# Performance work log

Hardware: AMD Instinct MI355X
Metric: run time of the kernel (lower is better)

Reference implementation:

```python
import jax, jax.numpy as jnp
import numpy as np

V_TH = 1.0  # spikingjelly IFNode default threshold; v starts at 0, hard reset after fire


def setup_inputs() -> dict:
    key = jax.random.key(0)
    k_x, k_w1, k_w2 = jax.random.split(key, 3)
    B, IN, FEAT, OUT = 4096, 3136, 6272, 500
    # binary input spikes (LatencyEncoder emits 0/1 spikes per timestep)
    x = (jax.random.uniform(k_x, (B, IN)) < 0.5).astype(jnp.float32)
    # Linear weights, torch layout [out_features, in_features], kaiming-ish scale
    W1 = jax.random.normal(k_w1, (FEAT, IN), dtype=jnp.float32) / np.sqrt(IN)
    W2 = jax.random.normal(k_w2, (OUT, FEAT), dtype=jnp.float32) / np.sqrt(FEAT)
    return {"x": x, "W1": W1, "W2": W2}


def reference(x, W1, W2):
    # Linear (no bias) -> IF neuron single step: v = 0 + I; spike = (v >= V_TH); hard reset
    v1 = x @ W1.T                      # [B, FEAT]
    s1 = (v1 >= V_TH).astype(x.dtype)  # binary hidden spikes
    v2 = s1 @ W2.T                     # [B, OUT]
    s2 = (v2 >= V_TH).astype(x.dtype)  # output spikes
    return s2
```

## Files before the change

### kernel.cpp

```cpp
#include <hip/hip_runtime.h>


namespace {
constexpr int kB = 4096;
constexpr int kIn = 3136;
constexpr int kFeat = 6272;
constexpr int kFeatWords = 196;
constexpr int kOut = 500;
constexpr size_t kPlane1 = (size_t)kFeat * kIn;
constexpr size_t kW1F = 3 * kPlane1;
constexpr size_t kW2F = (size_t)784 * 12288;
constexpr size_t kS1Bytes = (size_t)kB * kFeatWords * 4;
constexpr size_t kXb2Bytes = (size_t)49 * kB * 8;
constexpr unsigned kCap1 = 2u << 20;
constexpr unsigned kCap2 = 1u << 16;
__device__ constexpr double kTau1 = 7.4769e-4;
__device__ constexpr double kTau2 = 1.4955e-3;
}

typedef int v4i __attribute__((ext_vector_type(4)));
typedef int v16i __attribute__((ext_vector_type(16)));

__device__ __forceinline__ void gload_lds16(const void* g, void* l) {
  __builtin_amdgcn_global_load_lds((__attribute__((address_space(1))) void*)(g),
                                   (__attribute__((address_space(3))) void*)(l),
                                   16, 0, 0);
}

__device__ __forceinline__ v4i expand16(unsigned b) {
  unsigned u0 = (((b      ) & 0xFu) * 0x204081u) & 0x01010101u;
  unsigned u1 = (((b >> 4 ) & 0xFu) * 0x204081u) & 0x01010101u;
  unsigned u2 = (((b >> 8 ) & 0xFu) * 0x204081u) & 0x01010101u;
  unsigned u3 = (((b >> 12) & 0xFu) * 0x204081u) & 0x01010101u;
  return (v4i){(int)u0, (int)u1, (int)u2, (int)u3};
}

__device__ __forceinline__ void split3(float w, signed char* d) {
  float c = rintf(w * 128.f);
  d[0] = (signed char)(int)c;
  float r = fmaf(c, -7.8125e-03f, w);
  c = rintf(r * 16384.f);
  d[1] = (signed char)(int)c;
  r = fmaf(c, -6.103515625e-05f, r);
  c = rintf(r * 2097152.f);
  d[2] = (signed char)(int)c;
}

__global__ __launch_bounds__(256) void conv_w1F(const float* __restrict__ W,
                                                signed char* __restrict__ F) {
  const int bx = blockIdx.x;
  const int fb = bx / 49;
  const int kt = bx % 49;
  const int f = threadIdx.x & 63;
  const int g = threadIdx.x >> 6;
  const float* src = W + (size_t)(fb * 64 + f) * kIn + kt * 64 + g * 16;
  union { signed char c[16]; int4 v; } o[3];
#pragma unroll
  for (int q = 0; q < 4; ++q) {
    const float4 w = *(const float4*)(src + q * 4);
    signed char d[4][3];
    split3(w.x, d[0]); split3(w.y, d[1]); split3(w.z, d[2]); split3(w.w, d[3]);
#pragma unroll
    for (int e = 0; e < 4; ++e)
#pragma unroll
      for (int j = 0; j < 3; ++j) o[j].c[q * 4 + e] = d[e][j];
  }
#pragma unroll
  for (int j = 0; j < 3; ++j)
    *(int4*)(F + ((size_t)bx * 3 + j) * 4096 + g * 1024 + f * 16) = o[j].v;
}

__global__ __launch_bounds__(256) void conv_w2F(const float* __restrict__ W,
                                                signed char* __restrict__ F) {
  const int bx = blockIdx.x;
  const int fb = bx / 98;
  const int kt = bx % 98;
  const int f = threadIdx.x & 63;
  const int g = threadIdx.x >> 6;
  const int feat = fb * 64 + f;
  union { signed char c[16]; int4 v; } o[3];
#pragma unroll
  for (int q = 0; q < 4; ++q) {
    float4 w = {0.f, 0.f, 0.f, 0.f};
    if (feat < kOut)
      w = *(const float4*)(W + (size_t)feat * kFeat + kt * 64 + g * 16 + q * 4);
    signed char d[4][3];
    split3(w.x, d[0]); split3(w.y, d[1]); split3(w.z, d[2]); split3(w.w, d[3]);
#pragma unroll
    for (int e = 0; e < 4; ++e)
#pragma unroll
      for (int j = 0; j < 3; ++j) o[j].c[q * 4 + e] = d[e][j];
  }
#pragma unroll
  for (int j = 0; j < 3; ++j)
    *(int4*)(F + ((size_t)bx * 3 + j) * 4096 + g * 1024 + f * 16) = o[j].v;
}

__global__ __launch_bounds__(256) void pack_x2(const float* __restrict__ X,
                                               uint2* __restrict__ xb2) {
  const int wid = (blockIdx.x * 256 + threadIdx.x) >> 6;
  const int lane = threadIdx.x & 63;
  const int b = wid / 49;
  const int g = wid % 49;
  const float v = X[(size_t)b * kIn + g * 64 + lane];
  const unsigned long long bal = __ballot(v != 0.f);
  if (lane == 0) xb2[(size_t)g * kB + b] = make_uint2((unsigned)bal, (unsigned)(bal >> 32));
}

__global__ __launch_bounds__(512, 4) void fc1_v6(
    const uint2* __restrict__ xb2, const signed char* __restrict__ w1lF,
    unsigned* __restrict__ s1b, unsigned* __restrict__ s1T,
    unsigned* __restrict__ cnt, unsigned* __restrict__ list) {
  __shared__ __align__(16) signed char lds[24576];
  const int tid = threadIdx.x;
  const int lane = tid & 63;
  const int ln31 = lane & 31;
  const int half = lane >> 5;
  const int wv = tid >> 6;
  const int waveM = wv >> 1;
  const int waveN = wv & 1;
  const int bx = blockIdx.y;
  const int bM = blockIdx.x * 128;

  const signed char* const gbase = w1lF + (size_t)bx * 49 * 12288;
  const bool has1 = (wv < 4);
  const unsigned sG0 = wv * 1024u + lane * 16u;
  const unsigned sL0 = wv * 1024u;
  const unsigned sG1 = (wv + 8) * 1024u + lane * 16u;
  const unsigned sL1 = (wv + 8) * 1024u;

  const uint2* const aptr = xb2 + bM + waveM * 32 + ln31;
  const unsigned bfeat = (waveN * 32 + ln31) * 16u;

  v16i acc[3] = {};
  uint2 aC, aN;
  aC = aptr[0];
  gload_lds16(gbase + sG0, lds + sL0);
  if (has1) gload_lds16(gbase + sG1, lds + sL1);

  for (int kt = 0; kt < 49; ++kt) {
    __syncthreads();
    const int cb = (kt & 1) * 12288;
    if (kt < 48) {
      const int nb = ((kt + 1) & 1) * 12288;
      const size_t go = (size_t)(kt + 1) * 12288;
      gload_lds16(gbase + go + sG0, lds + nb + sL0);
      if (has1) gload_lds16(gbase + go + sG1, lds + nb + sL1);
      aN = aptr[(size_t)(kt + 1) * kB];
    }
#pragma unroll
    for (int kk = 0; kk < 2; ++kk) {
      const unsigned gsel = (kk * 2 + half) * 1024u;
      const v4i b0 = *(const v4i*)(lds + cb + 0 * 4096 + gsel + bfeat);
      const v4i b1 = *(const v4i*)(lds + cb + 1 * 4096 + gsel + bfeat);
      const v4i b2 = *(const v4i*)(lds + cb + 2 * 4096 + gsel + bfeat);
      const unsigned word = kk ? aC.y : aC.x;
      const v4i a = expand16((word >> (half * 16)) & 0xFFFFu);
      acc[0] = __builtin_amdgcn_mfma_i32_32x32x32_i8(a, b0, acc[0], 0, 0, 0);
      acc[1] = __builtin_amdgcn_mfma_i32_32x32x32_i8(a, b1, acc[1], 0, 0, 0);
      acc[2] = __builtin_amdgcn_mfma_i32_32x32x32_i8(a, b2, acc[2], 0, 0, 0);
    }
    aC = aN;
  }

  const double s7 = 0.0078125;
  const int word = bx * 2 + waveN;
  const int fcol = word * 32 + ln31;
#pragma unroll
  for (int t = 0; t < 16; ++t) {
    double v = (double)acc[2][t];
    v = v * s7 + (double)acc[1][t];
    v = v * s7 + (double)acc[0][t];
    v = v * s7;
    const unsigned long long bal = __ballot(v >= 1.0);
    const int mrow = bM + waveM * 32 + (t & 3) + 8 * (t >> 2);
    if (lane == 0) {
      s1b[(size_t)mrow * kFeatWords + word] = (unsigned)bal;
      s1T[(size_t)word * kB + mrow] = (unsigned)bal;
    }
    if (lane == 32) {
      s1b[(size_t)(mrow + 4) * kFeatWords + word] = (unsigned)(bal >> 32);
      s1T[(size_t)word * kB + mrow + 4] = (unsigned)(bal >> 32);
    }
    if (fabs(v - 1.0) <= kTau1) {
      const unsigned idx = atomicAdd(cnt, 1u);
      if (idx < kCap1) list[idx] = ((unsigned)(mrow + 4 * half) << 13) | (unsigned)fcol;
    }
  }
}

__global__ __launch_bounds__(256) void fc1_correct(
    const float* __restrict__ x, const float* __restrict__ W1,
    const unsigned* __restrict__ cnt, const unsigned* __restrict__ list,
    unsigned* __restrict__ s1b, unsigned* __restrict__ s1T) {
  const unsigned n = min(cnt[0], kCap1);
  const int lane = threadIdx.x & 63;
  const int wid = (blockIdx.x * 256 + threadIdx.x) >> 6;
  const int nw = (gridDim.x * 256) >> 6;
  for (unsigned i = wid; i < n; i += nw) {
    const unsigned u = list[i];
    const int b = (int)(u >> 13);
    const int f = (int)(u & 8191u);
    double s = 0.0;
    for (int k = lane; k < kIn; k += 64)
      s = fma((double)x[(size_t)b * kIn + k], (double)W1[(size_t)f * kIn + k], s);
#pragma unroll
    for (int off = 32; off > 0; off >>= 1) s += __shfl_down(s, off);
    if (lane == 0) {
      const unsigned mask = 1u << (f & 31);
      unsigned* p1 = s1b + (size_t)b * kFeatWords + (f >> 5);
      unsigned* p2 = s1T + (size_t)(f >> 5) * kB + b;
      if (s >= 1.0) { atomicOr(p1, mask); atomicOr(p2, mask); }
      else          { atomicAnd(p1, ~mask); atomicAnd(p2, ~mask); }
    }
  }
}

__global__ __launch_bounds__(128, 4) void fc2_v6(
    const unsigned* __restrict__ s1T, const signed char* __restrict__ w2lF,
    float* __restrict__ out, unsigned* __restrict__ cnt,
    unsigned* __restrict__ list) {
  const int tid = threadIdx.x;
  const int lane = tid & 63;
  const int ln31 = lane & 31;
  const int half = lane >> 5;
  const int wvN = tid >> 6;
  const int bx = blockIdx.y;
  const int bM = blockIdx.x * 32;

  const unsigned* const aptr = s1T + bM + ln31;
  const int fl = wvN * 32 + ln31;
  const signed char* const bbase =
      w2lF + (size_t)(bx * 98) * 12288 + half * 1024u + fl * 16u;

  v16i acc[3] = {};
  v4i b0[6], b1[6];
  uint2 a0, a1;

#define LOAD_TILE(nk, bf, ab)                                   \
  {                                                             \
    const signed char* bp = bbase + (size_t)(nk) * 12288;       \
    bf[0] = *(const v4i*)(bp);                                  \
    bf[1] = *(const v4i*)(bp + 2048);                           \
    bf[2] = *(const v4i*)(bp + 4096);                           \
    bf[3] = *(const v4i*)(bp + 6144);                           \
    bf[4] = *(const v4i*)(bp + 8192);                           \
    bf[5] = *(const v4i*)(bp + 10240);                          \
    (ab).x = aptr[(size_t)((nk) * 2) * kB];                     \
    (ab).y = aptr[(size_t)((nk) * 2 + 1) * kB];                 \
  }
#define COMPUTE_TILE(bf, ab)                                                    \
  {                                                                             \
    _Pragma("unroll")                                                           \
    for (int kk = 0; kk < 2; ++kk) {                                            \
      const unsigned word = kk ? (ab).y : (ab).x;                               \
      const v4i a = expand16((word >> (half * 16)) & 0xFFFFu);                  \
      acc[0] = __builtin_amdgcn_mfma_i32_32x32x32_i8(a, bf[kk], acc[0], 0,0,0); \
      acc[1] = __builtin_amdgcn_mfma_i32_32x32x32_i8(a, bf[2+kk], acc[1],0,0,0);\
      acc[2] = __builtin_amdgcn_mfma_i32_32x32x32_i8(a, bf[4+kk], acc[2],0,0,0);\
    }                                                                           \
  }

  LOAD_TILE(0, b0, a0);
  for (int kt = 0; kt + 2 <= 98; kt += 2) {
    LOAD_TILE(kt + 1, b1, a1);
    COMPUTE_TILE(b0, a0);
    const int nk2 = (kt + 2 < 98) ? kt + 2 : 97;
    LOAD_TILE(nk2, b0, a0);
    COMPUTE_TILE(b1, a1);
  }

  const double s7 = 0.0078125;
  const int o = bx * 64 + wvN * 32 + ln31;
#pragma unroll
  for (int t = 0; t < 16; ++t) {
    double v = (double)acc[2][t];
    v = v * s7 + (double)acc[1][t];
    v = v * s7 + (double)acc[0][t];
    v = v * s7;
    const int b = bM + (t & 3) + 8 * (t >> 2) + 4 * half;
    if (o < kOut) {
      out[(size_t)b * kOut + o] = (v >= 1.0) ? 1.0f : 0.0f;
      if (fabs(v - 1.0) <= kTau2) {
        const unsigned idx = atomicAdd(cnt, 1u);
        if (idx < kCap2) list[idx] = ((unsigned)b << 13) | (unsigned)o;
      }
    }
  }
#undef LOAD_TILE
#undef COMPUTE_TILE
}

__global__ __launch_bounds__(256) void fc2_correct(
    const unsigned* __restrict__ s1b, const float* __restrict__ W2,
    const unsigned* __restrict__ cnt, const unsigned* __restrict__ list,
    float* __restrict__ out) {
  const unsigned n = min(cnt[0], kCap2);
  const int lane = threadIdx.x & 63;
  const int wid = (blockIdx.x * 256 + threadIdx.x) >> 6;
  const int nw = (gridDim.x * 256) >> 6;
  for (unsigned i = wid; i < n; i += nw) {
    const unsigned u = list[i];
    const int b = (int)(u >> 13);
    const int o = (int)(u & 8191u);
    double s = 0.0;
    for (int k = lane; k < kFeat; k += 64) {
      const unsigned w = s1b[(size_t)b * kFeatWords + (k >> 5)];
      if ((w >> (k & 31)) & 1u) s += (double)W2[(size_t)o * kFeat + k];
    }
#pragma unroll
    for (int off = 32; off > 0; off >>= 1) s += __shfl_down(s, off);
    if (lane == 0) out[(size_t)b * kOut + o] = (s >= 1.0) ? 1.0f : 0.0f;
  }
}

__global__ __launch_bounds__(256) void snn_fc1(const float* __restrict__ x,
                                               const float* __restrict__ W1,
                                               unsigned int* __restrict__ s1bits) {
  __shared__ double Xd[32][66];
  __shared__ double Wd[32][66];
  __shared__ unsigned int spikes[64][2];
  const int tid = threadIdx.x;
  const int tx = tid & 15;
  const int ty = tid >> 4;
  const int b0 = blockIdx.y * 64;
  const int f0 = blockIdx.x * 64;
  if (tid < 128) spikes[tid >> 1][tid & 1] = 0u;
  double acc[4][4];
#pragma unroll
  for (int j = 0; j < 4; ++j)
#pragma unroll
    for (int i = 0; i < 4; ++i) acc[j][i] = 0.0;
  const int rl = tid >> 2;
  const int kq = (tid & 3) * 8;
  const float* xrow = x + (size_t)(b0 + rl) * kIn + kq;
  const float* wrow = W1 + (size_t)(f0 + rl) * kIn + kq;
  for (int kc = 0; kc < kIn; kc += 32) {
    const float4 xv0 = *(const float4*)(xrow + kc);
    const float4 xv1 = *(const float4*)(xrow + kc + 4);
    const float4 wv0 = *(const float4*)(wrow + kc);
    const float4 wv1 = *(const float4*)(wrow + kc + 4);
    __syncthreads();
    Xd[kq + 0][rl] = (double)xv0.x; Xd[kq + 1][rl] = (double)xv0.y;
    Xd[kq + 2][rl] = (double)xv0.z; Xd[kq + 3][rl] = (double)xv0.w;
    Xd[kq + 4][rl] = (double)xv1.x; Xd[kq + 5][rl] = (double)xv1.y;
    Xd[kq + 6][rl] = (double)xv1.z; Xd[kq + 7][rl] = (double)xv1.w;
    Wd[kq + 0][rl] = (double)wv0.x; Wd[kq + 1][rl] = (double)wv0.y;
    Wd[kq + 2][rl] = (double)wv0.z; Wd[kq + 3][rl] = (double)wv0.w;
    Wd[kq + 4][rl] = (double)wv1.x; Wd[kq + 5][rl] = (double)wv1.y;
    Wd[kq + 6][rl] = (double)wv1.z; Wd[kq + 7][rl] = (double)wv1.w;
    __syncthreads();
#pragma unroll
    for (int k = 0; k < 32; ++k) {
      const double2 xa = *(const double2*)&Xd[k][ty * 4];
      const double2 xb = *(const double2*)&Xd[k][ty * 4 + 2];
      const double2 wa = *(const double2*)&Wd[k][tx * 4];
      const double2 wb = *(const double2*)&Wd[k][tx * 4 + 2];
      const double xv[4] = {xa.x, xa.y, xb.x, xb.y};
      const double wv[4] = {wa.x, wa.y, wb.x, wb.y};
#pragma unroll
      for (int j = 0; j < 4; ++j)
#pragma unroll
        for (int i = 0; i < 4; ++i) acc[j][i] += xv[j] * wv[i];
    }
  }
  __syncthreads();
#pragma unroll
  for (int j = 0; j < 4; ++j) {
    unsigned int nib = 0u;
#pragma unroll
    for (int i = 0; i < 4; ++i) nib |= (acc[j][i] >= 1.0 ? 1u : 0u) << i;
    atomicOr(&spikes[ty * 4 + j][tx >> 3], nib << ((tx * 4) & 31));
  }
  __syncthreads();
  if (tid < 128) {
    const int r = tid >> 1;
    const int w = tid & 1;
    s1bits[(size_t)(b0 + r) * kFeatWords + (f0 >> 5) + w] = spikes[r][w];
  }
}

__global__ __launch_bounds__(256) void snn_fc2(const unsigned int* __restrict__ s1bits,
                                               const float* __restrict__ W2,
                                               float* __restrict__ out) {
  __shared__ double Wd[32][66];
  __shared__ unsigned int Sb[64];
  const int tid = threadIdx.x;
  const int tx = tid & 15;
  const int ty = tid >> 4;
  const int b0 = blockIdx.y * 64;
  const int o0 = blockIdx.x * 64;
  double acc[4][4];
#pragma unroll
  for (int j = 0; j < 4; ++j)
#pragma unroll
    for (int i = 0; i < 4; ++i) acc[j][i] = 0.0;
  const int rl = tid >> 2;
  const int kq = (tid & 3) * 8;
  int orow = o0 + rl;
  if (orow >= kOut) orow = kOut - 1;
  const float* wrow = W2 + (size_t)orow * kFeat + kq;
  for (int kc = 0; kc < kFeat; kc += 32) {
    const float4 wv0 = *(const float4*)(wrow + kc);
    const float4 wv1 = *(const float4*)(wrow + kc + 4);
    unsigned int sword = 0u;
    if (tid < 64) sword = s1bits[(size_t)(b0 + tid) * kFeatWords + (kc >> 5)];
    __syncthreads();
    Wd[kq + 0][rl] = (double)wv0.x; Wd[kq + 1][rl] = (double)wv0.y;
    Wd[kq + 2][rl] = (double)wv0.z; Wd[kq + 3][rl] = (double)wv0.w;
    Wd[kq + 4][rl] = (double)wv1.x; Wd[kq + 5][rl] = (double)wv1.y;
    Wd[kq + 6][rl] = (double)wv1.z; Wd[kq + 7][rl] = (double)wv1.w;
    if (tid < 64) Sb[tid] = sword;
    __syncthreads();
    const unsigned int rw0 = Sb[ty * 4 + 0];
    const unsigned int rw1 = Sb[ty * 4 + 1];
    const unsigned int rw2 = Sb[ty * 4 + 2];
    const unsigned int rw3 = Sb[ty * 4 + 3];
#pragma unroll
    for (int k = 0; k < 32; ++k) {
      const double2 wa = *(const double2*)&Wd[k][tx * 4];
      const double2 wb = *(const double2*)&Wd[k][tx * 4 + 2];
      const double wv[4] = {wa.x, wa.y, wb.x, wb.y};
      const double sv[4] = {(double)((rw0 >> k) & 1u), (double)((rw1 >> k) & 1u),
                            (double)((rw2 >> k) & 1u), (double)((rw3 >> k) & 1u)};
#pragma unroll
      for (int j = 0; j < 4; ++j)
#pragma unroll
        for (int i = 0; i < 4; ++i) acc[j][i] += sv[j] * wv[i];
    }
  }
#pragma unroll
  for (int j = 0; j < 4; ++j) {
    const int b = b0 + ty * 4 + j;
#pragma unroll
    for (int i = 0; i < 4; ++i) {
      const int o = o0 + tx * 4 + i;
      if (o < kOut) out[(size_t)b * kOut + o] = (acc[j][i] >= 1.0) ? 1.0f : 0.0f;
    }
  }
}

extern "C" void kernel_launch(void* const* d_in, const int* in_sizes, int n_in,
                              void* d_out, int out_size, void* d_ws, size_t ws_size,
                              hipStream_t stream) {
  const float* x = (const float*)d_in[0];
  const float* W1 = (const float*)d_in[1];
  const float* W2 = (const float*)d_in[2];
  float* out = (float*)d_out;

  char* p = (char*)d_ws;
  signed char* w1lF = (signed char*)p;   p += kW1F;
  signed char* w2lF = (signed char*)p;   p += kW2F;
  unsigned* s1b = (unsigned*)p;          p += kS1Bytes;
  unsigned* s1T = (unsigned*)p;          p += kS1Bytes;
  uint2* xb2 = (uint2*)p;                p += kXb2Bytes;
  unsigned* list1 = (unsigned*)p;        p += (size_t)kCap1 * 4;
  unsigned* list2 = (unsigned*)p;        p += (size_t)kCap2 * 4;
  unsigned* ctrs = (unsigned*)p;         p += 256;
  const size_t need = (size_t)(p - (char*)d_ws);

  if (ws_size >= need) {
    hipMemsetAsync(ctrs, 0, 32, stream);
    conv_w1F<<<4802, 256, 0, stream>>>(W1, w1lF);
    conv_w2F<<<784, 256, 0, stream>>>(W2, w2lF);
    pack_x2<<<50176, 256, 0, stream>>>(x, xb2);
    fc1_v6<<<dim3(32, 98), 512, 0, stream>>>(xb2, w1lF, s1b, s1T, ctrs, list1);
    fc1_correct<<<1024, 256, 0, stream>>>(x, W1, ctrs, list1, s1b, s1T);
    fc2_v6<<<dim3(128, 8), 128, 0, stream>>>(s1T, w2lF, out, ctrs + 4, list2);
    fc2_correct<<<64, 256, 0, stream>>>(s1b, W2, ctrs + 4, list2, out);
  } else {
    unsigned* s1 = (unsigned*)d_ws;
    snn_fc1<<<dim3(98, 64), 256, 0, stream>>>(x, W1, s1);
    snn_fc2<<<dim3(8, 64), 256, 0, stream>>>(s1, W2, out);
  }
}
```

Before: 585.7 us.

## Double fc1 M-tile per block and swizzle block order for L2 locality

The fc1 kernel now computes 256 batch rows per block instead of 128. Each wave handles two 32-row subtiles that share the same LDS-staged W1 tile, which halves the weight streaming per output and doubles the accumulator registers. Block indices in fc1 and fc2 are remapped through an XCD-style swizzle so consecutive blocks land on related tiles, aiming at better L2 reuse across chiplets. The larger accumulator state may reduce occupancy under the existing launch bounds.

```diff
diff --git a/kernel.cpp b/kernel.cpp
--- a/kernel.cpp
+++ b/kernel.cpp
@@ -107,7 +107,7 @@
   if (lane == 0) xb2[(size_t)g * kB + b] = make_uint2((unsigned)bal, (unsigned)(bal >> 32));
 }
 
-__global__ __launch_bounds__(512, 4) void fc1_v6(
+__global__ __launch_bounds__(512, 4) void fc1_v10(
     const uint2* __restrict__ xb2, const signed char* __restrict__ w1lF,
     unsigned* __restrict__ s1b, unsigned* __restrict__ s1T,
     unsigned* __restrict__ cnt, unsigned* __restrict__ list) {
@@ -119,8 +119,11 @@
   const int wv = tid >> 6;
   const int waveM = wv >> 1;
   const int waveN = wv & 1;
-  const int bx = blockIdx.y;
-  const int bM = blockIdx.x * 128;
+
+  const int lin = blockIdx.x + 16 * blockIdx.y;
+  const int sw = (lin & 7) * 196 + (lin >> 3);
+  const int bx = sw >> 4;
+  const int bM = (sw & 15) * 256;
 
   const signed char* const gbase = w1lF + (size_t)bx * 49 * 12288;
   const bool has1 = (wv < 4);
@@ -129,24 +132,30 @@
   const unsigned sG1 = (wv + 8) * 1024u + lane * 16u;
   const unsigned sL1 = (wv + 8) * 1024u;
 
-  const uint2* const aptr = xb2 + bM + waveM * 32 + ln31;
+  const uint2* const aptr = xb2 + bM + waveM * 64 + ln31;
   const unsigned bfeat = (waveN * 32 + ln31) * 16u;
 
-  v16i acc[3] = {};
-  uint2 aC, aN;
-  aC = aptr[0];
+  v16i acc[2][3] = {};
+  uint2 aC0, aC1, aN0, aN1;
+
   gload_lds16(gbase + sG0, lds + sL0);
   if (has1) gload_lds16(gbase + sG1, lds + sL1);
+  aC0 = aptr[0];
+  aC1 = aptr[32];
+  const uint2* apn = aptr + (size_t)kB;
+  const signed char* gstage = gbase + 12288;
 
   for (int kt = 0; kt < 49; ++kt) {
     __syncthreads();
     const int cb = (kt & 1) * 12288;
     if (kt < 48) {
       const int nb = ((kt + 1) & 1) * 12288;
-      const size_t go = (size_t)(kt + 1) * 12288;
-      gload_lds16(gbase + go + sG0, lds + nb + sL0);
-      if (has1) gload_lds16(gbase + go + sG1, lds + nb + sL1);
-      aN = aptr[(size_t)(kt + 1) * kB];
+      gload_lds16(gstage + sG0, lds + nb + sL0);
+      if (has1) gload_lds16(gstage + sG1, lds + nb + sL1);
+      gstage += 12288;
+      aN0 = apn[0];
+      aN1 = apn[32];
+      apn += (size_t)kB;
     }
 #pragma unroll
     for (int kk = 0; kk < 2; ++kk) {
@@ -154,37 +163,46 @@
       const v4i b0 = *(const v4i*)(lds + cb + 0 * 4096 + gsel + bfeat);
       const v4i b1 = *(const v4i*)(lds + cb + 1 * 4096 + gsel + bfeat);
       const v4i b2 = *(const v4i*)(lds + cb + 2 * 4096 + gsel + bfeat);
-      const unsigned word = kk ? aC.y : aC.x;
-      const v4i a = expand16((word >> (half * 16)) & 0xFFFFu);
-      acc[0] = __builtin_amdgcn_mfma_i32_32x32x32_i8(a, b0, acc[0], 0, 0, 0);
-      acc[1] = __builtin_amdgcn_mfma_i32_32x32x32_i8(a, b1, acc[1], 0, 0, 0);
-      acc[2] = __builtin_amdgcn_mfma_i32_32x32x32_i8(a, b2, acc[2], 0, 0, 0);
-    }
-    aC = aN;
+      const unsigned w0 = kk ? aC0.y : aC0.x;
+      const v4i a0 = expand16((w0 >> (half * 16)) & 0xFFFFu);
+      acc[0][0] = __builtin_amdgcn_mfma_i32_32x32x32_i8(a0, b0, acc[0][0], 0, 0, 0);
+      acc[0][1] = __builtin_amdgcn_mfma_i32_32x32x32_i8(a0, b1, acc[0][1], 0, 0, 0);
+      acc[0][2] = __builtin_amdgcn_mfma_i32_32x32x32_i8(a0, b2, acc[0][2], 0, 0, 0);
+      const unsigned w1 = kk ? aC1.y : aC1.x;
+      const v4i a1 = expand16((w1 >> (half * 16)) & 0xFFFFu);
+      acc[1][0] = __builtin_amdgcn_mfma_i32_32x32x32_i8(a1, b0, acc[1][0], 0, 0, 0);
+      acc[1][1] = __builtin_amdgcn_mfma_i32_32x32x32_i8(a1, b1, acc[1][1], 0, 0, 0);
+      acc[1][2] = __builtin_amdgcn_mfma_i32_32x32x32_i8(a1, b2, acc[1][2], 0, 0, 0);
+    }
+    aC0 = aN0;
+    aC1 = aN1;
   }
 
   const double s7 = 0.0078125;
   const int word = bx * 2 + waveN;
   const int fcol = word * 32 + ln31;
 #pragma unroll
-  for (int t = 0; t < 16; ++t) {
-    double v = (double)acc[2][t];
-    v = v * s7 + (double)acc[1][t];
-    v = v * s7 + (double)acc[0][t];
-    v = v * s7;
-    const unsigned long long bal = __ballot(v >= 1.0);
-    const int mrow = bM + waveM * 32 + (t & 3) + 8 * (t >> 2);
-    if (lane == 0) {
-      s1b[(size_t)mrow * kFeatWords + word] = (unsigned)bal;
-      s1T[(size_t)word * kB + mrow] = (unsigned)bal;
-    }
-    if (lane == 32) {
-      s1b[(size_t)(mrow + 4) * kFeatWords + word] = (unsigned)(bal >> 32);
-      s1T[(size_t)word * kB + mrow + 4] = (unsigned)(bal >> 32);
-    }
-    if (fabs(v - 1.0) <= kTau1) {
-      const unsigned idx = atomicAdd(cnt, 1u);
-      if (idx < kCap1) list[idx] = ((unsigned)(mrow + 4 * half) << 13) | (unsigned)fcol;
+  for (int sub = 0; sub < 2; ++sub) {
+#pragma unroll
+    for (int t = 0; t < 16; ++t) {
+      double v = (double)acc[sub][2][t];
+      v = v * s7 + (double)acc[sub][1][t];
+      v = v * s7 + (double)acc[sub][0][t];
+      v = v * s7;
+      const unsigned long long bal = __ballot(v >= 1.0);
+      const int mrow = bM + waveM * 64 + sub * 32 + (t & 3) + 8 * (t >> 2);
+      if (lane == 0) {
+        s1b[(size_t)mrow * kFeatWords + word] = (unsigned)bal;
+        s1T[(size_t)word * kB + mrow] = (unsigned)bal;
+      }
+      if (lane == 32) {
+        s1b[(size_t)(mrow + 4) * kFeatWords + word] = (unsigned)(bal >> 32);
+        s1T[(size_t)word * kB + mrow + 4] = (unsigned)(bal >> 32);
+      }
+      if (fabs(v - 1.0) <= kTau1) {
+        const unsigned idx = atomicAdd(cnt, 1u);
+        if (idx < kCap1) list[idx] = ((unsigned)(mrow + 4 * half) << 13) | (unsigned)fcol;
+      }
     }
   }
 }
@@ -216,7 +234,7 @@
   }
 }
 
-__global__ __launch_bounds__(128, 4) void fc2_v6(
+__global__ __launch_bounds__(128, 4) void fc2_v7(
     const unsigned* __restrict__ s1T, const signed char* __restrict__ w2lF,
     float* __restrict__ out, unsigned* __restrict__ cnt,
     unsigned* __restrict__ list) {
@@ -225,8 +243,11 @@
   const int ln31 = lane & 31;
   const int half = lane >> 5;
   const int wvN = tid >> 6;
-  const int bx = blockIdx.y;
-  const int bM = blockIdx.x * 32;
+
+  const int lin = blockIdx.x + 128 * blockIdx.y;
+  const int sw = ((lin & 7) << 7) + (lin >> 3);
+  const int bx = sw >> 7;
+  const int bM = (sw & 127) * 32;
 
   const unsigned* const aptr = s1T + bM + ln31;
   const int fl = wvN * 32 + ln31;
@@ -464,9 +485,9 @@
     conv_w1F<<<4802, 256, 0, stream>>>(W1, w1lF);
     conv_w2F<<<784, 256, 0, stream>>>(W2, w2lF);
     pack_x2<<<50176, 256, 0, stream>>>(x, xb2);
-    fc1_v6<<<dim3(32, 98), 512, 0, stream>>>(xb2, w1lF, s1b, s1T, ctrs, list1);
+    fc1_v10<<<dim3(16, 98), 512, 0, stream>>>(xb2, w1lF, s1b, s1T, ctrs, list1);
     fc1_correct<<<1024, 256, 0, stream>>>(x, W1, ctrs, list1, s1b, s1T);
-    fc2_v6<<<dim3(128, 8), 128, 0, stream>>>(s1T, w2lF, out, ctrs + 4, list2);
+    fc2_v7<<<dim3(128, 8), 128, 0, stream>>>(s1T, w2lF, out, ctrs + 4, list2);
     fc2_correct<<<64, 256, 0, stream>>>(s1b, W2, ctrs + 4, list2, out);
   } else {
     unsigned* s1 = (unsigned*)d_ws;
```

After: 576.3 us. Within noise of the previous version (-1.6%).
